# Optimization experiments

Measured on AMD Instinct MI355X. Metric: run time of the kernel, lower is better.

Reference implementation:

```python
import jax, jax.numpy as jnp
import numpy as np

NEG_SLOPE = 0.01  # F.leaky_relu default


def setup_inputs() -> dict:
    key = jax.random.key(0)
    k1, k2, k3, k4 = jax.random.split(key, 4)
    N, F, E = 50000, 64, 800000
    h = jax.random.normal(k1, (N, F), dtype=jnp.float32)
    # attn_fc: Linear(2F, 1, bias=False) -> weight vector of length 2F
    attn_w = jax.random.normal(k2, (2 * F,), dtype=jnp.float32) * (1.0 / np.sqrt(2 * F))
    src = jax.random.randint(k3, (E,), 0, N, dtype=jnp.int32)
    dst = jnp.sort(jax.random.randint(k4, (E,), 0, N, dtype=jnp.int32))
    return {"h": h, "attn_w": attn_w, "src": src, "dst": dst}


def reference(h, attn_w, src, dst):
    N, F = h.shape
    # gather per-edge src/dst features
    z_src = h[src]                      # [E, F]
    z_dst = h[dst]                      # [E, F]
    # cat([z_src, z_dst]) @ w  ==  z_src @ w[:F] + z_dst @ w[F:]
    e = z_src @ attn_w[:F] + z_dst @ attn_w[F:]          # [E]
    e = jnp.where(e >= 0, e, NEG_SLOPE * e)               # leaky_relu
    # segment softmax over incoming edges of each dst node (numerically stable)
    e_max = jax.ops.segment_max(e, dst, num_segments=N)   # [N], -inf for empty
    e_exp = jnp.exp(e - e_max[dst])                       # [E]
    denom = jax.ops.segment_sum(e_exp, dst, num_segments=N)  # [N]
    alpha = e_exp / denom[dst]                            # [E]
    # weighted scatter-sum of src features into dst nodes
    out = jax.ops.segment_sum(alpha[:, None] * z_src, dst, num_segments=N)  # [N, F]
    return out
```

## Files before the change

### kernel.cpp

```cpp
#include <hip/hip_runtime.h>
#include <math.h>

#define NEG_SLOPE 0.01f

__device__ __forceinline__ unsigned short f2bf_rne(float f) {
    unsigned int u = __float_as_uint(f);
    u += 0x7fffu + ((u >> 16) & 1u);
    return (unsigned short)(u >> 16);
}
__device__ __forceinline__ float bf2f(unsigned short b) {
    return __uint_as_float((unsigned int)b << 16);
}

__global__ void prep2(const float* __restrict__ h, const float* __restrict__ w,
                      const int* __restrict__ dst,
                      float* __restrict__ a_src, float* __restrict__ a_dst,
                      int* __restrict__ seg, ushort4* __restrict__ hb,
                      int N, int E, int PB) {
    if ((int)blockIdx.x < PB) {
        int gid  = blockIdx.x * blockDim.x + threadIdx.x;
        int node = gid >> 4, q = gid & 15;
        if (node >= N) return;
        float4 hv = *(const float4*)(h + (long)node * 64 + q * 4);
        float4 ws = *(const float4*)(w + q * 4);
        float4 wd = *(const float4*)(w + 64 + q * 4);
        ushort4 hb4 = { f2bf_rne(hv.x), f2bf_rne(hv.y), f2bf_rne(hv.z), f2bf_rne(hv.w) };
        hb[(long)node * 16 + q] = hb4;
        float ps = hv.x * ws.x + hv.y * ws.y + hv.z * ws.z + hv.w * ws.w;
        float pd = hv.x * wd.x + hv.y * wd.y + hv.z * wd.z + hv.w * wd.w;
        #pragma unroll
        for (int o = 8; o; o >>= 1) { ps += __shfl_xor(ps, o); pd += __shfl_xor(pd, o); }
        if (q == 0) { a_src[node] = ps; a_dst[node] = pd; }
    } else {
        int i = (blockIdx.x - PB) * blockDim.x + threadIdx.x;
        if (i >= E) return;
        int d    = dst[i];
        int prev = (i == 0) ? -1 : dst[i - 1];
        for (int n = prev + 1; n <= d; ++n) seg[n] = i;
        if (i == E - 1) {
            for (int n = d + 1; n <= N; ++n) seg[n] = E;
        }
    }
}

__global__ void gat_out(const ushort4* __restrict__ hb, const float* __restrict__ a_src,
                        const float* __restrict__ a_dst, const int* __restrict__ src,
                        const int* __restrict__ seg, float* __restrict__ out, int N) {
    int gid   = blockIdx.x * blockDim.x + threadIdx.x;
    int node  = gid >> 4;
    if (node >= N) return;
    int lane  = threadIdx.x & 63;
    int q     = lane & 15;
    int gbase = lane & 48;
    int s     = seg[node];
    int eend  = seg[node + 1];
    int deg   = eend - s;
    float* orow = out + (long)node * 64 + q * 4;

    int wdeg = deg;
    wdeg = max(wdeg, __shfl_xor(wdeg, 16));
    wdeg = max(wdeg, __shfl_xor(wdeg, 32));

    float ad = a_dst[node];
    float4 acc = {0.0f, 0.0f, 0.0f, 0.0f};
    const ushort4* hq = hb + q;

    if (wdeg <= 64) {
        int   sj0 = 0, sj1 = 0, sj2 = 0, sj3 = 0;
        float e0 = -INFINITY, e1 = -INFINITY, e2 = -INFINITY, e3 = -INFINITY;
        if (q < deg)      { sj0 = src[s + q];      float t = a_src[sj0] + ad; e0 = (t >= 0.f) ? t : NEG_SLOPE * t; }
        if (q + 16 < deg) { sj1 = src[s + q + 16]; float t = a_src[sj1] + ad; e1 = (t >= 0.f) ? t : NEG_SLOPE * t; }
        if (q + 32 < deg) { sj2 = src[s + q + 32]; float t = a_src[sj2] + ad; e2 = (t >= 0.f) ? t : NEG_SLOPE * t; }
        if (q + 48 < deg) { sj3 = src[s + q + 48]; float t = a_src[sj3] + ad; e3 = (t >= 0.f) ? t : NEG_SLOPE * t; }
        float m = fmaxf(fmaxf(e0, e1), fmaxf(e2, e3));
        #pragma unroll
        for (int o = 8; o; o >>= 1) m = fmaxf(m, __shfl_xor(m, o));
        float p0 = (q < deg)      ? __expf(e0 - m) : 0.0f;
        float p1 = (q + 16 < deg) ? __expf(e1 - m) : 0.0f;
        float p2 = (q + 32 < deg) ? __expf(e2 - m) : 0.0f;
        float p3 = (q + 48 < deg) ? __expf(e3 - m) : 0.0f;
        float dsum = p0 + p1 + p2 + p3;
        #pragma unroll
        for (int o = 8; o; o >>= 1) dsum += __shfl_xor(dsum, o);
        float inv = (dsum > 0.0f) ? (1.0f / dsum) : 0.0f;
        p0 *= inv; p1 *= inv; p2 *= inv; p3 *= inv;

        #define CHUNK(P, SJ, BASE)                                              \
        {   int cnt = wdeg - (BASE); cnt = (cnt > 16) ? 16 : cnt;               \
            _Pragma("unroll 8")                                                 \
            for (int j = 0; j < cnt; ++j) {                                     \
                float aj  = __shfl((P), gbase + j);                             \
                int   sjj = __shfl((SJ), gbase + j);                            \
                ushort4 hv = hq[(long)sjj * 16];                                \
                acc.x = fmaf(aj, bf2f(hv.x), acc.x);                            \
                acc.y = fmaf(aj, bf2f(hv.y), acc.y);                            \
                acc.z = fmaf(aj, bf2f(hv.z), acc.z);                            \
                acc.w = fmaf(aj, bf2f(hv.w), acc.w);                            \
            }                                                                   \
        }
        CHUNK(p0, sj0, 0)
        if (wdeg > 16) CHUNK(p1, sj1, 16)
        if (wdeg > 32) CHUNK(p2, sj2, 32)
        if (wdeg > 48) CHUNK(p3, sj3, 48)
        #undef CHUNK
        *(float4*)orow = acc;
    } else {
        float m = -INFINITY;
        for (int i = s + q; i < eend; i += 16) {
            float t = a_src[src[i]] + ad;
            t = (t >= 0.f) ? t : NEG_SLOPE * t;
            m = fmaxf(m, t);
        }
        #pragma unroll
        for (int o = 8; o; o >>= 1) m = fmaxf(m, __shfl_xor(m, o));
        float dsum = 0.0f;
        for (int i = s + q; i < eend; i += 16) {
            float t = a_src[src[i]] + ad;
            t = (t >= 0.f) ? t : NEG_SLOPE * t;
            dsum += __expf(t - m);
        }
        #pragma unroll
        for (int o = 8; o; o >>= 1) dsum += __shfl_xor(dsum, o);
        float inv = (dsum > 0.0f) ? (1.0f / dsum) : 0.0f;
        for (int i = s; i < eend; ++i) {
            int   sj = src[i];
            float t  = a_src[sj] + ad;
            t = (t >= 0.f) ? t : NEG_SLOPE * t;
            float aj = __expf(t - m) * inv;
            ushort4 hv = hq[(long)sj * 16];
            acc.x = fmaf(aj, bf2f(hv.x), acc.x);
            acc.y = fmaf(aj, bf2f(hv.y), acc.y);
            acc.z = fmaf(aj, bf2f(hv.z), acc.z);
            acc.w = fmaf(aj, bf2f(hv.w), acc.w);
        }
        *(float4*)orow = acc;
    }
}

extern "C" void kernel_launch(void* const* d_in, const int* in_sizes, int n_in,
                              void* d_out, int out_size, void* d_ws, size_t ws_size,
                              hipStream_t stream) {
    const float* h   = (const float*)d_in[0];
    const float* w   = (const float*)d_in[1];
    const int*   src = (const int*)d_in[2];
    const int*   dst = (const int*)d_in[3];
    float*       out = (float*)d_out;

    const int F = in_sizes[1] / 2;
    const int N = in_sizes[0] / F;
    const int E = in_sizes[2];

    char* wsb   = (char*)d_ws;
    float* a_src = (float*)wsb;
    float* a_dst = a_src + N;
    int*   seg   = (int*)(a_dst + N);
    size_t off   = ((size_t)(3 * N + 1) * 4 + 255) & ~(size_t)255;
    ushort4* hb  = (ushort4*)(wsb + off);

    const int PB = (N * 16 + 255) / 256;
    const int SB = (E + 255) / 256;
    prep2<<<dim3(PB + SB), dim3(256), 0, stream>>>(h, w, dst, a_src, a_dst, seg, hb, N, E, PB);
    gat_out<<<dim3((N * 16 + 255) / 256), dim3(256), 0, stream>>>(hb, a_src, a_dst, src, seg, out, N);
}
```

Baseline: 40.17 us.

## Precompute per-edge logits in separate kernel and batch gathers via shared memory

Splits the prep into a node kernel and a new edge kernel that computes leaky-relu logits per edge (coalesced, 4 edges per thread) and builds segment offsets, so the aggregation kernel reads e contiguously instead of gathering a_src per edge. The aggregation loop stages normalized weights and source indices in LDS and issues 8 independent row gathers before the FMAs, replacing serial shuffle-driven loads to raise memory-level parallelism. It costs an extra kernel launch, an E-sized workspace buffer write and read, and serializes prep before the edge kernel.

```diff
diff --git a/kernel.cpp b/kernel.cpp
--- a/kernel.cpp
+++ b/kernel.cpp
@@ -12,66 +12,85 @@
     return __uint_as_float((unsigned int)b << 16);
 }
 
-__global__ void prep2(const float* __restrict__ h, const float* __restrict__ w,
-                      const int* __restrict__ dst,
-                      float* __restrict__ a_src, float* __restrict__ a_dst,
-                      int* __restrict__ seg, ushort4* __restrict__ hb,
-                      int N, int E, int PB) {
-    if ((int)blockIdx.x < PB) {
-        int gid  = blockIdx.x * blockDim.x + threadIdx.x;
-        int node = gid >> 4, q = gid & 15;
-        if (node >= N) return;
-        float4 hv = *(const float4*)(h + (long)node * 64 + q * 4);
-        float4 ws = *(const float4*)(w + q * 4);
-        float4 wd = *(const float4*)(w + 64 + q * 4);
-        ushort4 hb4 = { f2bf_rne(hv.x), f2bf_rne(hv.y), f2bf_rne(hv.z), f2bf_rne(hv.w) };
-        hb[(long)node * 16 + q] = hb4;
-        float ps = hv.x * ws.x + hv.y * ws.y + hv.z * ws.z + hv.w * ws.w;
-        float pd = hv.x * wd.x + hv.y * wd.y + hv.z * wd.z + hv.w * wd.w;
-        #pragma unroll
-        for (int o = 8; o; o >>= 1) { ps += __shfl_xor(ps, o); pd += __shfl_xor(pd, o); }
-        if (q == 0) { a_src[node] = ps; a_dst[node] = pd; }
+__global__ void prep(const float* __restrict__ h, const float* __restrict__ w,
+                     float* __restrict__ a_src, float* __restrict__ a_dst,
+                     ushort4* __restrict__ hb, int N) {
+    int gid  = blockIdx.x * blockDim.x + threadIdx.x;
+    int node = gid >> 4, q = gid & 15;
+    if (node >= N) return;
+    float4 hv = *(const float4*)(h + (long)node * 64 + q * 4);
+    float4 ws = *(const float4*)(w + q * 4);
+    float4 wd = *(const float4*)(w + 64 + q * 4);
+    ushort4 hb4 = { f2bf_rne(hv.x), f2bf_rne(hv.y), f2bf_rne(hv.z), f2bf_rne(hv.w) };
+    hb[(long)node * 16 + q] = hb4;
+    float ps = hv.x * ws.x + hv.y * ws.y + hv.z * ws.z + hv.w * ws.w;
+    float pd = hv.x * wd.x + hv.y * wd.y + hv.z * wd.z + hv.w * wd.w;
+    #pragma unroll
+    for (int o = 8; o; o >>= 1) { ps += __shfl_xor(ps, o); pd += __shfl_xor(pd, o); }
+    if (q == 0) { a_src[node] = ps; a_dst[node] = pd; }
+}
+
+__global__ void edge_e(const int* __restrict__ src, const int* __restrict__ dst,
+                       const float* __restrict__ a_src, const float* __restrict__ a_dst,
+                       float* __restrict__ e, int* __restrict__ seg, int N, int E) {
+    int i0 = (blockIdx.x * blockDim.x + threadIdx.x) * 4;
+    if (i0 >= E) return;
+    if (i0 + 4 <= E) {
+        int4 s4 = *(const int4*)(src + i0);
+        int4 d4 = *(const int4*)(dst + i0);
+        int prev = (i0 == 0) ? -1 : dst[i0 - 1];
+        float4 ev; float t;
+        t = a_src[s4.x] + a_dst[d4.x]; ev.x = (t >= 0.f) ? t : NEG_SLOPE * t;
+        t = a_src[s4.y] + a_dst[d4.y]; ev.y = (t >= 0.f) ? t : NEG_SLOPE * t;
+        t = a_src[s4.z] + a_dst[d4.z]; ev.z = (t >= 0.f) ? t : NEG_SLOPE * t;
+        t = a_src[s4.w] + a_dst[d4.w]; ev.w = (t >= 0.f) ? t : NEG_SLOPE * t;
+        *(float4*)(e + i0) = ev;
+        for (int n = prev + 1; n <= d4.x; ++n) seg[n] = i0;
+        for (int n = d4.x + 1; n <= d4.y; ++n) seg[n] = i0 + 1;
+        for (int n = d4.y + 1; n <= d4.z; ++n) seg[n] = i0 + 2;
+        for (int n = d4.z + 1; n <= d4.w; ++n) seg[n] = i0 + 3;
+        if (i0 + 4 == E) { for (int n = d4.w + 1; n <= N; ++n) seg[n] = E; }
     } else {
-        int i = (blockIdx.x - PB) * blockDim.x + threadIdx.x;
-        if (i >= E) return;
-        int d    = dst[i];
-        int prev = (i == 0) ? -1 : dst[i - 1];
-        for (int n = prev + 1; n <= d; ++n) seg[n] = i;
-        if (i == E - 1) {
-            for (int n = d + 1; n <= N; ++n) seg[n] = E;
+        for (int i = i0; i < E; ++i) {
+            int sj = src[i], dj = dst[i];
+            int prev = (i == 0) ? -1 : dst[i - 1];
+            float t = a_src[sj] + a_dst[dj];
+            e[i] = (t >= 0.f) ? t : NEG_SLOPE * t;
+            for (int n = prev + 1; n <= dj; ++n) seg[n] = i;
+            if (i == E - 1) { for (int n = dj + 1; n <= N; ++n) seg[n] = E; }
         }
     }
 }
 
-__global__ void gat_out(const ushort4* __restrict__ hb, const float* __restrict__ a_src,
-                        const float* __restrict__ a_dst, const int* __restrict__ src,
-                        const int* __restrict__ seg, float* __restrict__ out, int N) {
-    int gid   = blockIdx.x * blockDim.x + threadIdx.x;
-    int node  = gid >> 4;
+__global__ void gat_out(const ushort4* __restrict__ hb, const float* __restrict__ e,
+                        const int* __restrict__ src, const int* __restrict__ seg,
+                        float* __restrict__ out, int N) {
+    int gid  = blockIdx.x * blockDim.x + threadIdx.x;
+    int node = gid >> 4;
     if (node >= N) return;
-    int lane  = threadIdx.x & 63;
-    int q     = lane & 15;
-    int gbase = lane & 48;
-    int s     = seg[node];
-    int eend  = seg[node + 1];
-    int deg   = eend - s;
+    int tid  = threadIdx.x;
+    int lane = tid & 63, q = lane & 15, g = (lane >> 4) & 3, wv = tid >> 6;
+    int s    = seg[node];
+    int eend = seg[node + 1];
+    int deg  = eend - s;
     float* orow = out + (long)node * 64 + q * 4;
+
+    __shared__ float2 pair[4][4][66];
 
     int wdeg = deg;
     wdeg = max(wdeg, __shfl_xor(wdeg, 16));
     wdeg = max(wdeg, __shfl_xor(wdeg, 32));
 
-    float ad = a_dst[node];
+    const ushort4* hq = hb + q;
     float4 acc = {0.0f, 0.0f, 0.0f, 0.0f};
-    const ushort4* hq = hb + q;
 
     if (wdeg <= 64) {
+        float e0 = -INFINITY, e1 = -INFINITY, e2 = -INFINITY, e3 = -INFINITY;
         int   sj0 = 0, sj1 = 0, sj2 = 0, sj3 = 0;
-        float e0 = -INFINITY, e1 = -INFINITY, e2 = -INFINITY, e3 = -INFINITY;
-        if (q < deg)      { sj0 = src[s + q];      float t = a_src[sj0] + ad; e0 = (t >= 0.f) ? t : NEG_SLOPE * t; }
-        if (q + 16 < deg) { sj1 = src[s + q + 16]; float t = a_src[sj1] + ad; e1 = (t >= 0.f) ? t : NEG_SLOPE * t; }
-        if (q + 32 < deg) { sj2 = src[s + q + 32]; float t = a_src[sj2] + ad; e2 = (t >= 0.f) ? t : NEG_SLOPE * t; }
-        if (q + 48 < deg) { sj3 = src[s + q + 48]; float t = a_src[sj3] + ad; e3 = (t >= 0.f) ? t : NEG_SLOPE * t; }
+        if (q < deg)      { e0 = e[s + q];      sj0 = src[s + q]; }
+        if (q + 16 < deg) { e1 = e[s + q + 16]; sj1 = src[s + q + 16]; }
+        if (q + 32 < deg) { e2 = e[s + q + 32]; sj2 = src[s + q + 32]; }
+        if (q + 48 < deg) { e3 = e[s + q + 48]; sj3 = src[s + q + 48]; }
         float m = fmaxf(fmaxf(e0, e1), fmaxf(e2, e3));
         #pragma unroll
         for (int o = 8; o; o >>= 1) m = fmaxf(m, __shfl_xor(m, o));
@@ -83,50 +102,46 @@
         #pragma unroll
         for (int o = 8; o; o >>= 1) dsum += __shfl_xor(dsum, o);
         float inv = (dsum > 0.0f) ? (1.0f / dsum) : 0.0f;
-        p0 *= inv; p1 *= inv; p2 *= inv; p3 *= inv;
 
-        #define CHUNK(P, SJ, BASE)                                              \
-        {   int cnt = wdeg - (BASE); cnt = (cnt > 16) ? 16 : cnt;               \
-            _Pragma("unroll 8")                                                 \
-            for (int j = 0; j < cnt; ++j) {                                     \
-                float aj  = __shfl((P), gbase + j);                             \
-                int   sjj = __shfl((SJ), gbase + j);                            \
-                ushort4 hv = hq[(long)sjj * 16];                                \
-                acc.x = fmaf(aj, bf2f(hv.x), acc.x);                            \
-                acc.y = fmaf(aj, bf2f(hv.y), acc.y);                            \
-                acc.z = fmaf(aj, bf2f(hv.z), acc.z);                            \
-                acc.w = fmaf(aj, bf2f(hv.w), acc.w);                            \
-            }                                                                   \
+        float2* gp = pair[wv][g];
+        gp[q]      = make_float2(p0 * inv, __int_as_float(sj0));
+        gp[q + 16] = make_float2(p1 * inv, __int_as_float(sj1));
+        gp[q + 32] = make_float2(p2 * inv, __int_as_float(sj2));
+        gp[q + 48] = make_float2(p3 * inv, __int_as_float(sj3));
+
+        int dr = (deg + 7) & ~7;
+        for (int j0 = 0; j0 < dr; j0 += 8) {
+            float a_[8]; int s_[8];
+            #pragma unroll
+            for (int k = 0; k < 8; ++k) {
+                float2 pr = gp[j0 + k];
+                a_[k] = pr.x; s_[k] = __float_as_int(pr.y);
+            }
+            ushort4 r_[8];
+            #pragma unroll
+            for (int k = 0; k < 8; ++k) r_[k] = hq[(long)s_[k] * 16];
+            #pragma unroll
+            for (int k = 0; k < 8; ++k) {
+                acc.x = fmaf(a_[k], bf2f(r_[k].x), acc.x);
+                acc.y = fmaf(a_[k], bf2f(r_[k].y), acc.y);
+                acc.z = fmaf(a_[k], bf2f(r_[k].z), acc.z);
+                acc.w = fmaf(a_[k], bf2f(r_[k].w), acc.w);
+            }
         }
-        CHUNK(p0, sj0, 0)
-        if (wdeg > 16) CHUNK(p1, sj1, 16)
-        if (wdeg > 32) CHUNK(p2, sj2, 32)
-        if (wdeg > 48) CHUNK(p3, sj3, 48)
-        #undef CHUNK
         *(float4*)orow = acc;
     } else {
         float m = -INFINITY;
-        for (int i = s + q; i < eend; i += 16) {
-            float t = a_src[src[i]] + ad;
-            t = (t >= 0.f) ? t : NEG_SLOPE * t;
-            m = fmaxf(m, t);
-        }
+        for (int i = s + q; i < eend; i += 16) m = fmaxf(m, e[i]);
         #pragma unroll
         for (int o = 8; o; o >>= 1) m = fmaxf(m, __shfl_xor(m, o));
         float dsum = 0.0f;
-        for (int i = s + q; i < eend; i += 16) {
-            float t = a_src[src[i]] + ad;
-            t = (t >= 0.f) ? t : NEG_SLOPE * t;
-            dsum += __expf(t - m);
-        }
+        for (int i = s + q; i < eend; i += 16) dsum += __expf(e[i] - m);
         #pragma unroll
         for (int o = 8; o; o >>= 1) dsum += __shfl_xor(dsum, o);
         float inv = (dsum > 0.0f) ? (1.0f / dsum) : 0.0f;
         for (int i = s; i < eend; ++i) {
+            float aj = __expf(e[i] - m) * inv;
             int   sj = src[i];
-            float t  = a_src[sj] + ad;
-            t = (t >= 0.f) ? t : NEG_SLOPE * t;
-            float aj = __expf(t - m) * inv;
             ushort4 hv = hq[(long)sj * 16];
             acc.x = fmaf(aj, bf2f(hv.x), acc.x);
             acc.y = fmaf(aj, bf2f(hv.y), acc.y);
@@ -150,15 +165,15 @@
     const int N = in_sizes[0] / F;
     const int E = in_sizes[2];
 
-    char* wsb   = (char*)d_ws;
+    char*  wsb   = (char*)d_ws;
     float* a_src = (float*)wsb;
     float* a_dst = a_src + N;
     int*   seg   = (int*)(a_dst + N);
-    size_t off   = ((size_t)(3 * N + 1) * 4 + 255) & ~(size_t)255;
+    float* ebuf  = (float*)(seg + N + 1);
+    size_t off   = (((size_t)(3 * N + 1) + E) * 4 + 255) & ~(size_t)255;
     ushort4* hb  = (ushort4*)(wsb + off);
 
-    const int PB = (N * 16 + 255) / 256;
-    const int SB = (E + 255) / 256;
-    prep2<<<dim3(PB + SB), dim3(256), 0, stream>>>(h, w, dst, a_src, a_dst, seg, hb, N, E, PB);
-    gat_out<<<dim3((N * 16 + 255) / 256), dim3(256), 0, stream>>>(hb, a_src, a_dst, src, seg, out, N);
+    prep   <<<dim3((N * 16 + 255) / 256), dim3(256), 0, stream>>>(h, w, a_src, a_dst, hb, N);
+    edge_e <<<dim3((E / 4 + 255) / 256), dim3(256), 0, stream>>>(src, dst, a_src, a_dst, ebuf, seg, N, E);
+    gat_out<<<dim3((N * 16 + 255) / 256), dim3(256), 0, stream>>>(hb, ebuf, src, seg, out, N);
 }
```

After: 35.74 us. 11.0% less time.
